# Optimization experiments

Measured on AMD Instinct MI355X. Metric: run time of the kernel, lower is better.

Reference implementation:

```python
import jax
import jax.numpy as jnp
import numpy as np
from jax import lax

NUM_POINT = 1024  # S


def farthest_point_sample(xyz, num_point):
    """D-FPS as in PointNet++ furthest_point_sample.

    xyz: (B, N, 3) float. Returns indices (B, S) int32.
    Iteratively picks the point farthest (in squared L2 over xyz) from the
    already-selected set, maintaining a running min-distance buffer.
    First selected index is 0 (matches the CUDA op's convention).
    """
    B, N, _ = xyz.shape

    def step(carry, _):
        dists, cur = carry  # dists: (B, N) running min sq-dist; cur: (B,) current idx
        cur_xyz = jnp.take_along_axis(xyz, cur[:, None, None], axis=1)  # (B, 1, 3)
        d = jnp.sum((xyz - cur_xyz) ** 2, axis=-1)  # (B, N)
        dists = jnp.minimum(dists, d)
        nxt = jnp.argmax(dists, axis=-1).astype(jnp.int32)  # farthest point
        return (dists, nxt), cur  # emit the index selected at this step

    init = (jnp.full((B, N), 1e10, dtype=xyz.dtype), jnp.zeros((B,), jnp.int32))
    _, idxs = lax.scan(step, init, None, length=num_point)  # idxs: (S, B)
    return idxs.T  # (B, S)


def setup_inputs() -> dict:
    key = jax.random.key(0)
    k1, k2 = jax.random.split(key)
    B, N, C = 8, 32768, 96
    points_xyz = jax.random.normal(k1, (B, N, 3), dtype=jnp.float32)
    features = jax.random.normal(k2, (B, C, N), dtype=jnp.float32)
    return {"points_xyz": points_xyz, "features": features}


def reference(points_xyz, features):
    # D-FPS sampling -> gather xyz and features by the sampled indices
    indices = farthest_point_sample(points_xyz, NUM_POINT)  # (B, S)
    # gather_points(xyz_flipped, idx).transpose -> (B, S, 3)
    new_xyz = jnp.take_along_axis(points_xyz, indices[:, :, None], axis=1)  # (B, S, 3)
    # gather_points(features, idx) -> (B, C, S)
    new_fea = jnp.take_along_axis(features, indices[:, None, :], axis=2)  # (B, C, S)
    return new_xyz, new_fea, indices
```

## Files before the change

### kernel.cpp

```cpp
#include <hip/hip_runtime.h>

#define B_ 8
#define N_ 32768
#define S_ 1024
#define C_ 96
#define P_ 2
#define T_ 512
#define W_ (T_ / 64)
#define HALF (N_ / P_)
#define PPT (HALF / T_)
#define NQ (PPT / 4)
#define PRS (PPT / 2)

typedef float f2v __attribute__((ext_vector_type(2)));
typedef unsigned long long u64;
typedef unsigned int u32;



#define U64_DPP_MAX(k, ctrl)                                                \
  {                                                                         \
    const u32 lo_ = (u32)(k), hi_ = (u32)((k) >> 32);                       \
    const u32 nlo_ = (u32)__builtin_amdgcn_update_dpp(                      \
        (int)lo_, (int)lo_, (ctrl), 0xf, 0xf, false);                       \
    const u32 nhi_ = (u32)__builtin_amdgcn_update_dpp(                      \
        (int)hi_, (int)hi_, (ctrl), 0xf, 0xf, false);                       \
    const u64 ok_ = ((u64)nhi_ << 32) | nlo_;                               \
    if (ok_ > (k)) (k) = ok_;                                               \
  }

__device__ __forceinline__ u64 ld_sc0(const u64* p) {
  u64 v;
  asm volatile("global_load_dwordx2 %0, %1, off sc0\n\t"
               "s_waitcnt vmcnt(0)"
               : "=v"(v) : "v"(p) : "memory");
  return v;
}

__global__ __launch_bounds__(T_)
__attribute__((amdgpu_waves_per_eu(2, 2)))
void fps_kernel(
    const float* __restrict__ xyz,
    float* __restrict__ out,
    u64* __restrict__ partsA,
    u64* __restrict__ partsL)
{
#pragma clang fp contract(off)
  const int blk  = blockIdx.x;
  const int b    = blk & 7;
  const int m    = blk >> 3;
  const int t    = threadIdx.x;
  const int lane = t & 63;
  const int w    = t >> 6;
  const float* xb = xyz + (size_t)b * N_ * 3;
  const int base = m * HALF;

  float* out_xyz = out;
  float* out_idx = out + (size_t)B_*S_*3 + (size_t)B_*C_*S_;

  __shared__ u64 red[2][W_];

  f2v XR[PRS], YR[PRS], ZR[PRS], Dr[PRS];
  #pragma unroll
  for (int k = 0; k < PRS; ++k) {
    const int g0 = base + (2*k)   * T_ + t;
    const int g1 = base + (2*k+1) * T_ + t;
    XR[k] = (f2v){xb[g0*3+0], xb[g1*3+0]};
    YR[k] = (f2v){xb[g0*3+1], xb[g1*3+1]};
    ZR[k] = (f2v){xb[g0*3+2], xb[g1*3+2]};
    Dr[k] = (f2v){1e10f, 1e10f};
  }
  #pragma unroll
  for (int k = 0; k < PRS; ++k) {
    asm volatile("" : "+v"(XR[k]), "+v"(YR[k]), "+v"(ZR[k]));
  }

  bool fastmode = true;
  int cur = 0;
  for (int s = 0; s < S_; ++s) {
    const int cu = __builtin_amdgcn_readfirstlane(cur);
    const float cx = xb[cu*3+0];
    const float cy = xb[cu*3+1];
    const float cz = xb[cu*3+2];
    if (m == 0 && t == 0) {
      out_idx[(size_t)b*S_ + s] = (float)cu;
      float* o = out_xyz + ((size_t)b*S_ + s)*3;
      o[0] = cx; o[1] = cy; o[2] = cz;
    }
    const f2v c2x = (f2v){cx, cx};
    const f2v c2y = (f2v){cy, cy};
    const f2v c2z = (f2v){cz, cz};

    float bv = -1.0f;
    int   bq = 0;
    f2v nw01 = (f2v){0.f, 0.f}, nw23 = (f2v){0.f, 0.f};

    #define UQ(qc)                                                         \
      {                                                                    \
        const f2v dx0 = XR[2*(qc)]   - c2x;                                \
        const f2v dy0 = YR[2*(qc)]   - c2y;                                \
        const f2v dz0 = ZR[2*(qc)]   - c2z;                                \
        const f2v d0  = (dx0*dx0 + dy0*dy0) + dz0*dz0;                     \
        const f2v dx1 = XR[2*(qc)+1] - c2x;                                \
        const f2v dy1 = YR[2*(qc)+1] - c2y;                                \
        const f2v dz1 = ZR[2*(qc)+1] - c2z;                                \
        const f2v d1  = (dx1*dx1 + dy1*dy1) + dz1*dz1;                     \
        const f2v nd0 = __builtin_elementwise_min(Dr[2*(qc)],   d0);       \
        const f2v nd1 = __builtin_elementwise_min(Dr[2*(qc)+1], d1);       \
        Dr[2*(qc)]   = nd0;                                                \
        Dr[2*(qc)+1] = nd1;                                                \
        const f2v qm2 = __builtin_elementwise_max(nd0, nd1);               \
        const float qm = fmaxf(qm2.x, qm2.y);                              \
        if (qm > bv) { bv = qm; bq = (qc); nw01 = nd0; nw23 = nd1; }       \
      }
    #pragma unroll
    for (int q = 0; q < NQ; ++q) { UQ(q); }
    #undef UQ

    int e = 3;
    if (nw23.x == bv) e = 2;
    if (nw01.y == bv) e = 1;
    if (nw01.x == bv) e = 0;
    const int bj = (bq << 2) + e;
    const int bg = base + (bj << 9) + t;

    u64 key = ((u64)__float_as_uint(bv) << 32) | (u32)(~bg);
    U64_DPP_MAX(key, 0x111);
    U64_DPP_MAX(key, 0x112);
    U64_DPP_MAX(key, 0x114);
    U64_DPP_MAX(key, 0x118);
    U64_DPP_MAX(key, 0x142);
    U64_DPP_MAX(key, 0x143);
    if (lane == 63) red[s & 1][w] = key;
    __syncthreads();

    u64 k = red[s & 1][lane & (W_ - 1)];
    U64_DPP_MAX(k, 0x111);
    U64_DPP_MAX(k, 0x112);
    U64_DPP_MAX(k, 0x114);
    const u32 klo = (u32)__builtin_amdgcn_readlane((int)(u32)k, 7);
    const u32 khi = (u32)__builtin_amdgcn_readlane((int)(k >> 32), 7);
    const u64 kblk = ((u64)khi << 32) | klo;

    u64* rowA = partsA + ((size_t)(b * S_ + s) << 1);
    u64* rowL = partsL + ((size_t)(b * S_ + s) << 1);
    if (t == 0) {
      __hip_atomic_store(&rowL[m], kblk, __ATOMIC_RELAXED,
                         __HIP_MEMORY_SCOPE_WORKGROUP);
      __hip_atomic_store(&rowA[m], kblk, __ATOMIC_RELAXED,
                         __HIP_MEMORY_SCOPE_AGENT);
    }
    u64 ko = 0;
    if (fastmode) {
      const int tries = (s == 0) ? 256 : 12;
      for (int i = 0; i < tries; ++i) {
        ko = ld_sc0(rowL + (1 - m));
        if (__ballot(ko != 0) == ~0ull) break;
      }
      if (__ballot(ko != 0) != ~0ull) { fastmode = false; ko = 0; }
    }
    if (ko == 0) {
      do {
        ko = __hip_atomic_load(&rowA[1 - m], __ATOMIC_RELAXED,
                               __HIP_MEMORY_SCOPE_AGENT);
      } while (__ballot(ko != 0) != ~0ull);
    }
    const u64 kw = (ko > kblk) ? ko : kblk;
    cur = (int)(u32)(~(u32)kw);
  }
}

__global__ void gather_fea_kernel(
    const float* __restrict__ feat,
    const float* __restrict__ idxf,
    float* __restrict__ out_fea)
{
  const int t = blockIdx.x * blockDim.x + threadIdx.x;
  if (t >= B_ * C_ * S_) return;
  const int s  = t & (S_ - 1);
  const int bc = t >> 10;
  const int c  = bc % C_;
  const int b  = bc / C_;
  const int idx = (int)idxf[(size_t)b * S_ + s];
  out_fea[t] = feat[((size_t)b * C_ + c) * (size_t)N_ + idx];
}

extern "C" void kernel_launch(void* const* d_in, const int* in_sizes, int n_in,
                              void* d_out, int out_size, void* d_ws, size_t ws_size,
                              hipStream_t stream) {
  const float* xyz  = (const float*)d_in[0];
  const float* feat = (const float*)d_in[1];
  float* out = (float*)d_out;

  float* out_fea = out + (size_t)B_ * S_ * 3;
  float* out_idx = out + (size_t)B_ * S_ * 3 + (size_t)B_ * C_ * S_;
  (void)d_ws; (void)ws_size; (void)in_sizes; (void)n_in; (void)out_size;

  u64* partsA = (u64*)out_fea;
  u64* partsL = partsA + (size_t)B_ * S_ * P_;
  hipMemsetAsync(partsA, 0, (size_t)2 * B_ * S_ * P_ * sizeof(u64), stream);

  fps_kernel<<<B_ * P_, T_, 0, stream>>>(xyz, out, partsA, partsL);

  const int total = B_ * C_ * S_;
  gather_fea_kernel<<<(total + 255) / 256, 256, 0, stream>>>(feat, out_idx, out_fea);
}
```

Baseline: 2.109 ms.

## Split each batch across four XCC-aware blocks with cross-block argmax exchange

Each batch's FPS is now split across four workgroups instead of two, which halves the points each thread handles per iteration. Blocks read their XCC id, publish it, and rank themselves so that the four blocks of a batch land on the same XCC where possible. That lets them exchange partial argmax keys through workgroup-scope (L2-local) stores, and the agent-scope path remains as a fallback. Wave 1 publishes the block's key while wave 0 polls the other three and reduces the result, which adds a second __syncthreads per step and more cross-block synchronization.

```diff
diff --git a/kernel.cpp b/kernel.cpp
--- a/kernel.cpp
+++ b/kernel.cpp
@@ -4,13 +4,14 @@
 #define N_ 32768
 #define S_ 1024
 #define C_ 96
-#define P_ 2
+#define P_ 4
 #define T_ 512
 #define W_ (T_ / 64)
-#define HALF (N_ / P_)
-#define PPT (HALF / T_)
+#define QTR (N_ / P_)
+#define PPT (QTR / T_)
 #define NQ (PPT / 4)
 #define PRS (PPT / 2)
+#define NBLK (B_ * P_)
 
 typedef float f2v __attribute__((ext_vector_type(2)));
 typedef unsigned long long u64;
@@ -43,22 +44,45 @@
     const float* __restrict__ xyz,
     float* __restrict__ out,
     u64* __restrict__ partsA,
-    u64* __restrict__ partsL)
+    u64* __restrict__ partsL,
+    u64* __restrict__ disc)
 {
 #pragma clang fp contract(off)
   const int blk  = blockIdx.x;
-  const int b    = blk & 7;
-  const int m    = blk >> 3;
   const int t    = threadIdx.x;
   const int lane = t & 63;
   const int w    = t >> 6;
-  const float* xb = xyz + (size_t)b * N_ * 3;
-  const int base = m * HALF;
 
   float* out_xyz = out;
   float* out_idx = out + (size_t)B_*S_*3 + (size_t)B_*C_*S_;
 
   __shared__ u64 red[2][W_];
+  __shared__ u64 winq[2];
+
+  u32 xcc;
+  asm volatile("s_getreg_b32 %0, hwreg(HW_REG_XCC_ID)" : "=s"(xcc));
+  if (t == 0) {
+    __hip_atomic_store(&disc[blk], (u64)(xcc + 1), __ATOMIC_RELAXED,
+                       __HIP_MEMORY_SCOPE_AGENT);
+  }
+  u64 dv;
+  do {
+    dv = __hip_atomic_load(&disc[lane & 31], __ATOMIC_RELAXED,
+                           __HIP_MEMORY_SCOPE_AGENT);
+  } while (__ballot(dv != 0) != ~0ull);
+  const int xl = (int)dv - 1;
+  const u64 M32 = 0xFFFFFFFFull;
+  const int idx = lane & 31;
+  const int Pn  = (int)__popcll(__ballot(xl < (int)xcc) & M32);
+  const int Cn  = (int)__popcll(__ballot(xl == (int)xcc) & M32);
+  const int rin = (int)__popcll(__ballot(xl == (int)xcc && idx < blk) & M32);
+  const int rank  = Pn + rin;
+  const int batch = rank >> 2;
+  const int mq    = rank & 3;
+  const bool fast_ok = (4*batch >= Pn) && (4*batch + 4 <= Pn + Cn);
+
+  const float* xb = xyz + (size_t)batch * N_ * 3;
+  const int base = mq * QTR;
 
   f2v XR[PRS], YR[PRS], ZR[PRS], Dr[PRS];
   #pragma unroll
@@ -75,16 +99,16 @@
     asm volatile("" : "+v"(XR[k]), "+v"(YR[k]), "+v"(ZR[k]));
   }
 
-  bool fastmode = true;
+  bool fastm = fast_ok;
   int cur = 0;
   for (int s = 0; s < S_; ++s) {
     const int cu = __builtin_amdgcn_readfirstlane(cur);
     const float cx = xb[cu*3+0];
     const float cy = xb[cu*3+1];
     const float cz = xb[cu*3+2];
-    if (m == 0 && t == 0) {
-      out_idx[(size_t)b*S_ + s] = (float)cu;
-      float* o = out_xyz + ((size_t)b*S_ + s)*3;
+    if (mq == 0 && t == 0) {
+      out_idx[(size_t)batch*S_ + s] = (float)cu;
+      float* o = out_xyz + ((size_t)batch*S_ + s)*3;
       o[0] = cx; o[1] = cy; o[2] = cz;
     }
     const f2v c2x = (f2v){cx, cx};
@@ -134,39 +158,57 @@
     if (lane == 63) red[s & 1][w] = key;
     __syncthreads();
 
-    u64 k = red[s & 1][lane & (W_ - 1)];
-    U64_DPP_MAX(k, 0x111);
-    U64_DPP_MAX(k, 0x112);
-    U64_DPP_MAX(k, 0x114);
-    const u32 klo = (u32)__builtin_amdgcn_readlane((int)(u32)k, 7);
-    const u32 khi = (u32)__builtin_amdgcn_readlane((int)(k >> 32), 7);
-    const u64 kblk = ((u64)khi << 32) | klo;
-
-    u64* rowA = partsA + ((size_t)(b * S_ + s) << 1);
-    u64* rowL = partsL + ((size_t)(b * S_ + s) << 1);
-    if (t == 0) {
-      __hip_atomic_store(&rowL[m], kblk, __ATOMIC_RELAXED,
-                         __HIP_MEMORY_SCOPE_WORKGROUP);
-      __hip_atomic_store(&rowA[m], kblk, __ATOMIC_RELAXED,
-                         __HIP_MEMORY_SCOPE_AGENT);
+    u64* rowA = partsA + ((size_t)(batch * S_ + s) << 2);
+    u64* rowL = partsL + ((size_t)(batch * S_ + s) << 4);
+
+    if (w < 2) {
+      u64 k = red[s & 1][lane & (W_ - 1)];
+      U64_DPP_MAX(k, 0x111);
+      U64_DPP_MAX(k, 0x112);
+      U64_DPP_MAX(k, 0x114);
+      const u32 klo = (u32)__builtin_amdgcn_readlane((int)(u32)k, 7);
+      const u32 khi = (u32)__builtin_amdgcn_readlane((int)(k >> 32), 7);
+      const u64 kblk = ((u64)khi << 32) | klo;
+
+      if (w == 1) {
+        if (lane == 0) {
+          if (fast_ok) {
+            __hip_atomic_store(&rowL[mq], kblk, __ATOMIC_RELAXED,
+                               __HIP_MEMORY_SCOPE_WORKGROUP);
+          }
+          __hip_atomic_store(&rowA[mq], kblk, __ATOMIC_RELAXED,
+                             __HIP_MEMORY_SCOPE_AGENT);
+        }
+      } else {
+        u64 ko = 0;
+        bool got = false;
+        if (fastm) {
+          const int tries = (s == 0) ? 512 : 32;
+          for (int i = 0; i < tries; ++i) {
+            u64 vv = ld_sc0(rowL + (lane & 3));
+            if ((lane & 3) == mq) vv = kblk;
+            ko = vv;
+            if (__ballot(ko != 0) == ~0ull) { got = true; break; }
+          }
+          if (!got) fastm = false;
+        }
+        if (!got) {
+          do {
+            ko = __hip_atomic_load(&rowA[lane & 3], __ATOMIC_RELAXED,
+                                   __HIP_MEMORY_SCOPE_AGENT);
+            if ((lane & 3) == mq) ko = kblk;
+          } while (__ballot(ko != 0) != ~0ull);
+        }
+        u64 kw = (ko > kblk) ? ko : kblk;
+        U64_DPP_MAX(kw, 0x111);
+        U64_DPP_MAX(kw, 0x112);
+        const u32 wlo = (u32)__builtin_amdgcn_readlane((int)(u32)kw, 3);
+        const u32 whi = (u32)__builtin_amdgcn_readlane((int)(kw >> 32), 3);
+        if (lane == 0) winq[s & 1] = ((u64)whi << 32) | wlo;
+      }
     }
-    u64 ko = 0;
-    if (fastmode) {
-      const int tries = (s == 0) ? 256 : 12;
-      for (int i = 0; i < tries; ++i) {
-        ko = ld_sc0(rowL + (1 - m));
-        if (__ballot(ko != 0) == ~0ull) break;
-      }
-      if (__ballot(ko != 0) != ~0ull) { fastmode = false; ko = 0; }
-    }
-    if (ko == 0) {
-      do {
-        ko = __hip_atomic_load(&rowA[1 - m], __ATOMIC_RELAXED,
-                               __HIP_MEMORY_SCOPE_AGENT);
-      } while (__ballot(ko != 0) != ~0ull);
-    }
-    const u64 kw = (ko > kblk) ? ko : kblk;
-    cur = (int)(u32)(~(u32)kw);
+    __syncthreads();
+    cur = (int)(u32)(~(u32)winq[s & 1]);
   }
 }
 
@@ -197,10 +239,12 @@
   (void)d_ws; (void)ws_size; (void)in_sizes; (void)n_in; (void)out_size;
 
   u64* partsA = (u64*)out_fea;
-  u64* partsL = partsA + (size_t)B_ * S_ * P_;
-  hipMemsetAsync(partsA, 0, (size_t)2 * B_ * S_ * P_ * sizeof(u64), stream);
-
-  fps_kernel<<<B_ * P_, T_, 0, stream>>>(xyz, out, partsA, partsL);
+  u64* partsL = partsA + (size_t)B_ * S_ * 4;
+  u64* disc   = partsL + (size_t)B_ * S_ * 16;
+  hipMemsetAsync(partsA, 0,
+                 ((size_t)B_ * S_ * 20 + NBLK) * sizeof(u64), stream);
+
+  fps_kernel<<<NBLK, T_, 0, stream>>>(xyz, out, partsA, partsL, disc);
 
   const int total = B_ * C_ * S_;
   gather_fea_kernel<<<(total + 255) / 256, 256, 0, stream>>>(feat, out_idx, out_fea);
```

New measurement: 1.904 ms. -9.7%, faster.
